# Kernel optimization log

Hardware: AMD Instinct MI355X
Metric: run time of the kernel (lower is better)

## Reference

```python
import jax, jax.numpy as jnp
import numpy as np

N_NODES = 50000
N_EDGES = 500000
MUL0, MUL1 = 16, 8          # multiplicities of 0e and 1o irreps (in == out)
DIM = MUL0 + 3 * MUL1       # 40
N_BASIS, MID = 10, 32
WNUM = MUL0*MUL0 + MUL1*MUL0 + MUL0*MUL1 + MUL1*MUL1  # 576
INV_SQRT3 = 1.0 / np.sqrt(3.0)  # wigner-3j normalization for l=1 paths
FAN_IN = MUL0 + MUL1        # paths into each output irrep: 16 + 8 = 24
A0 = np.sqrt(1.0 / FAN_IN)  # sqrt((2*0+1)/fan_in)
A1 = np.sqrt(3.0 / FAN_IN)  # sqrt((2*1+1)/fan_in)
LN_EPS = 1e-5


def setup_inputs() -> dict:
    key = jax.random.key(0)
    ks = jax.random.split(key, 8)
    return {
        "x": jax.random.normal(ks[0], (N_NODES, DIM), jnp.float32),
        "edge_sh": jax.random.normal(ks[1], (N_EDGES, 4), jnp.float32),
        "edge_length_embedded": jax.random.uniform(ks[2], (N_EDGES, N_BASIS), jnp.float32),
        "W1": jax.random.normal(ks[3], (N_BASIS, MID), jnp.float32),
        "W2": jax.random.normal(ks[4], (MID, WNUM), jnp.float32),
        "gamma": jnp.ones((DIM,), jnp.float32),
        "beta": jnp.zeros((DIM,), jnp.float32),
        "edge_src": jax.random.randint(ks[5], (N_EDGES,), 0, N_NODES),
        "edge_dst": jax.random.randint(ks[6], (N_EDGES,), 0, N_NODES),
        "avg_num_neighbors": 10,
    }


def reference(x, edge_sh, edge_length_embedded, W1, W2, gamma, beta,
              edge_src, edge_dst, avg_num_neighbors):
    # radial MLP -> per-edge tensor-product weights (e3nn FullyConnectedNet style)
    h = jax.nn.silu(edge_length_embedded @ W1 / jnp.sqrt(jnp.float32(N_BASIS)))
    w = h @ W2 / jnp.sqrt(jnp.float32(MID))              # [E, 576]

    # gather node features onto edges and split into irrep blocks
    xg = x[edge_src]                                     # [E, 40]
    s = xg[:, :MUL0]                                     # [E, 16]  scalars 0e
    v = xg[:, MUL0:].reshape(-1, MUL1, 3)                # [E, 8, 3] vectors 1o
    sh0 = edge_sh[:, 0]                                  # [E]
    sh1 = edge_sh[:, 1:4]                                # [E, 3]

    # split per-edge weights by tensor-product path
    o0, o1, o2 = MUL0*MUL0, MUL0*MUL0 + MUL1*MUL0, MUL0*MUL0 + MUL1*MUL0 + MUL0*MUL1
    W_ss0 = w[:, :o0].reshape(-1, MUL0, MUL0)            # 0e x 0e -> 0e
    W_vv0 = w[:, o0:o1].reshape(-1, MUL1, MUL0)          # 1o x 1o -> 0e
    W_sv1 = w[:, o1:o2].reshape(-1, MUL0, MUL1)          # 0e x 1o -> 1o
    W_vs1 = w[:, o2:].reshape(-1, MUL1, MUL1)            # 1o x 0e -> 1o

    # weighted Clebsch-Gordan tensor product (per edge)
    vdot = jnp.einsum('eui,ei->eu', v, sh1) * INV_SQRT3  # CG 1x1->0
    out0 = A0 * (jnp.einsum('euk,eu->ek', W_ss0, s * sh0[:, None])
                 + jnp.einsum('euk,eu->ek', W_vv0, vdot))            # [E, 16]
    out1 = A1 * INV_SQRT3 * (
        jnp.einsum('euk,eu->ek', W_sv1, s)[:, :, None] * sh1[:, None, :]
        + jnp.einsum('euk,eui->eki', W_vs1, v) * sh0[:, None, None])  # [E, 8, 3]
    edge_values = jnp.concatenate([out0, out1.reshape(-1, 3 * MUL1)], axis=1)

    # scatter-sum into destination nodes, degree normalization, layernorm
    node = jax.ops.segment_sum(edge_values, edge_dst, num_segments=N_NODES)
    node = node / jnp.sqrt(jnp.float32(avg_num_neighbors))
    mu = node.mean(axis=-1, keepdims=True)
    var = node.var(axis=-1, keepdims=True)
    return (node - mu) * jax.lax.rsqrt(var + LN_EPS) * gamma + beta
```

## Files before the change

kernel.cpp:

```cpp
#include <hip/hip_runtime.h>
#include <hip/hip_bf16.h>

#define N_NODES 50000
#define N_EDGES 500000
#define MUL0 16
#define MUL1 8
#define DIM 40
#define N_BASIS 10
#define MID 32
#define WNUM 576
#define SCAN_BLOCKS 196
#define N_GROUPS (N_EDGES / 16)

typedef __attribute__((ext_vector_type(8))) short bf16x8_t;
typedef __attribute__((ext_vector_type(4))) float f32x4_t;

__device__ __forceinline__ float bf2f(unsigned short u) {
  return __uint_as_float(((unsigned int)u) << 16);
}
__device__ __forceinline__ unsigned short f2bf(float f) {
  unsigned int x = __float_as_uint(f);
  unsigned int r = x + 0x7fffu + ((x >> 16) & 1u);
  return (unsigned short)(r >> 16);
}
__device__ __forceinline__ bool detect_bf16(const void* gamma) {
  return ((const unsigned int*)gamma)[0] == 0x3F803F80u;
}
template <bool BF16>
__device__ __forceinline__ float ld(const void* p, size_t i) {
  if (BF16) return bf2f(((const unsigned short*)p)[i]);
  return ((const float*)p)[i];
}

#define C_INV_SQRT10 0.31622776601683794f
#define C_INV_SQRT32 0.17677669529663687f
#define C_INV_SQRT3  0.5773502691896258f
#define C_A0C        0.20412414523193154f

__device__ __forceinline__ f32x4_t mfma16x16x32(bf16x8_t a, bf16x8_t b, f32x4_t c) {
  return __builtin_amdgcn_mfma_f32_16x16x32_bf16(a, b, c, 0, 0, 0);
}


__global__ __launch_bounds__(256) void hist_kernel(
    const int* __restrict__ edge_dst, int* __restrict__ cnt) {
  int e = blockIdx.x * 256 + threadIdx.x;
  if (e < N_EDGES) atomicAdd(&cnt[edge_dst[e]], 1);
}

__global__ __launch_bounds__(256) void scanA_kernel(
    const int* __restrict__ cnt, int* __restrict__ off, int* __restrict__ btot) {
  __shared__ int s[256];
  const int tid = threadIdx.x;
  const int i = blockIdx.x * 256 + tid;
  int v = (i < N_NODES) ? cnt[i] : 0;
  s[tid] = v;
  __syncthreads();
  for (int d = 1; d < 256; d <<= 1) {
    int t = (tid >= d) ? s[tid - d] : 0;
    __syncthreads();
    s[tid] += t;
    __syncthreads();
  }
  if (i < N_NODES) off[i] = s[tid] - v;
  if (tid == 255) btot[blockIdx.x] = s[255];
}

__global__ __launch_bounds__(256) void scanB_kernel(
    const int* __restrict__ btot, int* __restrict__ bbase) {
  __shared__ int s[256];
  const int tid = threadIdx.x;
  int v = (tid < SCAN_BLOCKS) ? btot[tid] : 0;
  s[tid] = v;
  __syncthreads();
  for (int d = 1; d < 256; d <<= 1) {
    int t = (tid >= d) ? s[tid - d] : 0;
    __syncthreads();
    s[tid] += t;
    __syncthreads();
  }
  if (tid < SCAN_BLOCKS) bbase[tid] = s[tid] - v;
}

__global__ __launch_bounds__(256) void scanC_kernel(
    int* __restrict__ off, const int* __restrict__ bbase) {
  const int i = blockIdx.x * 256 + threadIdx.x;
  if (i < N_NODES) off[i] += bbase[blockIdx.x];
}

__global__ __launch_bounds__(256) void pos_kernel(
    const int* __restrict__ edge_dst, const int* __restrict__ off,
    int* __restrict__ fill, int* __restrict__ epos) {
  int e = blockIdx.x * 256 + threadIdx.x;
  if (e >= N_EDGES) return;
  int d = edge_dst[e];
  epos[e] = off[d] + atomicAdd(&fill[d], 1);
}


template <bool BF16>
__device__ void edge_mfma_body(
    const void* __restrict__ x,
    const void* __restrict__ edge_sh,
    const void* __restrict__ elemb,
    const void* __restrict__ W1,
    const void* __restrict__ W2,
    const int* __restrict__ edge_src,
    const int* __restrict__ epos,
    unsigned short* __restrict__ ev,
    short* __restrict__ w2b, float* __restrict__ w1s, float* __restrict__ stg)
{
  const int tid = threadIdx.x;

  for (int i = tid; i < 36 * 512; i += 256) {
    int m = i / WNUM;
    int col = i - m * WNUM;
    int q = m >> 3, j = m & 7;
    int t = col >> 4, n = col & 15;
    short val;
    if (BF16) val = (short)((const unsigned short*)W2)[i];
    else      val = (short)f2bf(((const float*)W2)[i]);
    w2b[t * 512 + q * 128 + n * 8 + j] = val;
  }
  for (int i = tid; i < N_BASIS * MID; i += 256) w1s[i] = ld<BF16>(W1, i);
  __syncthreads();

  const int lane = tid & 63;
  const int wid  = tid >> 6;
  const int quad = lane >> 4;
  const int l16  = lane & 15;
  float* S = stg + wid * 832;

  for (int gi = blockIdx.x * 4 + wid; gi < N_GROUPS; gi += gridDim.x * 4) {
    const int e0 = gi * 16;
    __builtin_amdgcn_wave_barrier();

    const int posA = epos[e0 + (lane >> 2)];
    const int posB = (lane < 16) ? epos[e0 + lane] : 0;

    if (lane < 16) {
      if (BF16) {
        uint2 sw = *reinterpret_cast<const uint2*>(
            (const unsigned short*)edge_sh + (size_t)(e0 + lane) * 4);
        S[0 * 16 + lane] = __uint_as_float(sw.x << 16);
        S[1 * 16 + lane] = __uint_as_float(sw.x & 0xffff0000u);
        S[2 * 16 + lane] = __uint_as_float(sw.y << 16);
        S[3 * 16 + lane] = __uint_as_float(sw.y & 0xffff0000u);
      } else {
        float4 s4 = *reinterpret_cast<const float4*>(
            (const float*)edge_sh + (size_t)(e0 + lane) * 4);
        S[0 * 16 + lane] = s4.x; S[1 * 16 + lane] = s4.y;
        S[2 * 16 + lane] = s4.z; S[3 * 16 + lane] = s4.w;
      }
    }

    {
      const int src = edge_src[e0 + l16];
      if (BF16) {
        const uint4* xr = reinterpret_cast<const uint4*>(
            (const unsigned short*)x + (size_t)src * DIM);
        uint4 c = xr[quad];
        unsigned wv[4] = {c.x, c.y, c.z, c.w};
        #pragma unroll
        for (int p = 0; p < 4; ++p) {
          int col = quad * 8 + 2 * p;
          float lo = __uint_as_float(wv[p] << 16);
          float hi = __uint_as_float(wv[p] & 0xffff0000u);
          int off0 = (col < 16) ? (64 + col * 16) : (448 + (col - 16) * 16);
          int off1 = (col + 1 < 16) ? (64 + (col + 1) * 16) : (448 + (col - 15) * 16);
          S[off0 + l16] = lo;
          S[off1 + l16] = hi;
        }
        if (lane < 16) {
          uint4 c4 = xr[4];
          unsigned wv4[4] = {c4.x, c4.y, c4.z, c4.w};
          #pragma unroll
          for (int p = 0; p < 4; ++p) {
            int col = 32 + 2 * p;
            S[448 + (col - 16) * 16 + lane] = __uint_as_float(wv4[p] << 16);
            S[448 + (col - 15) * 16 + lane] = __uint_as_float(wv4[p] & 0xffff0000u);
          }
        }
      } else {
        const float4* xr = reinterpret_cast<const float4*>(
            (const float*)x + (size_t)src * DIM);
        #pragma unroll
        for (int cc = 0; cc < 2; ++cc) {
          int c = quad + cc * 4;
          float4 t = xr[c];
          float vv[4] = {t.x, t.y, t.z, t.w};
          #pragma unroll
          for (int p = 0; p < 4; ++p) {
            int col = 4 * c + p;
            int offp = (col < 16) ? (64 + col * 16) : (448 + (col - 16) * 16);
            S[offp + l16] = vv[p];
          }
        }
        if (quad < 2) {
          int c = 8 + quad;
          float4 t = xr[c];
          float vv[4] = {t.x, t.y, t.z, t.w};
          #pragma unroll
          for (int p = 0; p < 4; ++p) {
            int col = 4 * c + p;
            S[448 + (col - 16) * 16 + l16] = vv[p];
          }
        }
      }
    }
    __builtin_amdgcn_wave_barrier();

    #pragma unroll
    for (int p = 0; p < 2; ++p) {
      int idx = lane + p * 64;
      int u = idx >> 4, e = idx & 15;
      float vdv = (S[448 + (u * 3 + 0) * 16 + e] * S[16 + e] +
                   S[448 + (u * 3 + 1) * 16 + e] * S[32 + e] +
                   S[448 + (u * 3 + 2) * 16 + e] * S[48 + e]) * C_INV_SQRT3;
      S[320 + u * 16 + e] = vdv;
    }
    __builtin_amdgcn_wave_barrier();

    bf16x8_t af;
    {
      float eb[N_BASIS];
      if (BF16) {
        const unsigned short* er = (const unsigned short*)elemb + (size_t)(e0 + l16) * N_BASIS;
        #pragma unroll
        for (int p = 0; p < 5; ++p) {
          unsigned uv = *reinterpret_cast<const unsigned*>(er + p * 2);
          eb[2 * p]     = __uint_as_float(uv << 16);
          eb[2 * p + 1] = __uint_as_float(uv & 0xffff0000u);
        }
      } else {
        const float* er = (const float*)elemb + (size_t)(e0 + l16) * N_BASIS;
        #pragma unroll
        for (int p = 0; p < 5; ++p) {
          float2 fv = *reinterpret_cast<const float2*>(er + p * 2);
          eb[2 * p] = fv.x; eb[2 * p + 1] = fv.y;
        }
      }
      #pragma unroll
      for (int j = 0; j < 8; ++j) {
        int k = quad * 8 + j;
        float p = 0.f;
        #pragma unroll
        for (int b = 0; b < N_BASIS; ++b) p += eb[b] * w1s[b * MID + k];
        float z = p * C_INV_SQRT10;
        float hh = z / (1.f + __expf(-z)) * C_INV_SQRT32;
        af[j] = (short)f2bf(hh);
      }
    }

    f32x4_t s0 = *reinterpret_cast<const f32x4_t*>(&S[quad * 4]);

    f32x4_t out0 = {0.f, 0.f, 0.f, 0.f};
    f32x4_t tsv  = {0.f, 0.f, 0.f, 0.f};
    f32x4_t tv0  = {0.f, 0.f, 0.f, 0.f};
    f32x4_t tv1  = {0.f, 0.f, 0.f, 0.f};
    f32x4_t tv2  = {0.f, 0.f, 0.f, 0.f};
    const f32x4_t zero = {0.f, 0.f, 0.f, 0.f};
    const int usel = (l16 >> 3);

    #pragma unroll
    for (int t = 0; t < 16; ++t) {
      bf16x8_t bf = *reinterpret_cast<const bf16x8_t*>(&w2b[t * 512 + lane * 8]);
      f32x4_t D = mfma16x16x32(af, bf, zero);
      f32x4_t sv = *reinterpret_cast<const f32x4_t*>(&S[64 + t * 16 + quad * 4]);
      out0 += D * (sv * s0);
    }
    #pragma unroll
    for (int t = 0; t < 8; ++t) {
      bf16x8_t bf = *reinterpret_cast<const bf16x8_t*>(&w2b[(16 + t) * 512 + lane * 8]);
      f32x4_t D = mfma16x16x32(af, bf, zero);
      f32x4_t vdv = *reinterpret_cast<const f32x4_t*>(&S[320 + t * 16 + quad * 4]);
      out0 += D * vdv;
    }
    #pragma unroll
    for (int t = 0; t < 8; ++t) {
      bf16x8_t bf = *reinterpret_cast<const bf16x8_t*>(&w2b[(24 + t) * 512 + lane * 8]);
      f32x4_t D = mfma16x16x32(af, bf, zero);
      int u = 2 * t + usel;
      f32x4_t sv = *reinterpret_cast<const f32x4_t*>(&S[64 + u * 16 + quad * 4]);
      tsv += D * sv;
    }
    #pragma unroll
    for (int t = 0; t < 4; ++t) {
      bf16x8_t bf = *reinterpret_cast<const bf16x8_t*>(&w2b[(32 + t) * 512 + lane * 8]);
      f32x4_t D = mfma16x16x32(af, bf, zero);
      int u = 2 * t + usel;
      f32x4_t v0 = *reinterpret_cast<const f32x4_t*>(&S[448 + (u * 3 + 0) * 16 + quad * 4]);
      f32x4_t v1 = *reinterpret_cast<const f32x4_t*>(&S[448 + (u * 3 + 1) * 16 + quad * 4]);
      f32x4_t v2 = *reinterpret_cast<const f32x4_t*>(&S[448 + (u * 3 + 2) * 16 + quad * 4]);
      tv0 += D * v0; tv1 += D * v1; tv2 += D * v2;
    }

    #pragma unroll
    for (int r = 0; r < 4; ++r) {
      tsv[r] += __shfl_xor(tsv[r], 8, 64);
      tv0[r] += __shfl_xor(tv0[r], 8, 64);
      tv1[r] += __shfl_xor(tv1[r], 8, 64);
      tv2[r] += __shfl_xor(tv2[r], 8, 64);
    }
    __builtin_amdgcn_wave_barrier();

    #pragma unroll
    for (int r = 0; r < 4; ++r)
      S[64 + (quad * 4 + r) * 42 + l16] = C_A0C * out0[r];
    if (l16 < 8) {
      f32x4_t h1x = *reinterpret_cast<const f32x4_t*>(&S[16 + quad * 4]);
      f32x4_t h1y = *reinterpret_cast<const f32x4_t*>(&S[32 + quad * 4]);
      f32x4_t h1z = *reinterpret_cast<const f32x4_t*>(&S[48 + quad * 4]);
      #pragma unroll
      for (int r = 0; r < 4; ++r) {
        int rowb = 64 + (quad * 4 + r) * 42 + 16 + 3 * l16;
        S[rowb + 0] = C_A0C * (tsv[r] * h1x[r] + tv0[r] * s0[r]);
        S[rowb + 1] = C_A0C * (tsv[r] * h1y[r] + tv1[r] * s0[r]);
        S[rowb + 2] = C_A0C * (tsv[r] * h1z[r] + tv2[r] * s0[r]);
      }
    }
    __builtin_amdgcn_wave_barrier();

    {
      const int edge = lane >> 2, chunk = lane & 3;
      const float* rp = &S[64 + edge * 42 + chunk * 8];
      unsigned p0 = (unsigned)f2bf(rp[0]) | ((unsigned)f2bf(rp[1]) << 16);
      unsigned p1 = (unsigned)f2bf(rp[2]) | ((unsigned)f2bf(rp[3]) << 16);
      unsigned p2 = (unsigned)f2bf(rp[4]) | ((unsigned)f2bf(rp[5]) << 16);
      unsigned p3 = (unsigned)f2bf(rp[6]) | ((unsigned)f2bf(rp[7]) << 16);
      uint4 t; t.x = p0; t.y = p1; t.z = p2; t.w = p3;
      *reinterpret_cast<uint4*>(ev + (size_t)posA * DIM + chunk * 8) = t;
      if (lane < 16) {
        const float* rq = &S[64 + lane * 42 + 32];
        unsigned q0 = (unsigned)f2bf(rq[0]) | ((unsigned)f2bf(rq[1]) << 16);
        unsigned q1 = (unsigned)f2bf(rq[2]) | ((unsigned)f2bf(rq[3]) << 16);
        unsigned q2 = (unsigned)f2bf(rq[4]) | ((unsigned)f2bf(rq[5]) << 16);
        unsigned q3 = (unsigned)f2bf(rq[6]) | ((unsigned)f2bf(rq[7]) << 16);
        uint4 t2; t2.x = q0; t2.y = q1; t2.z = q2; t2.w = q3;
        *reinterpret_cast<uint4*>(ev + (size_t)posB * DIM + 32) = t2;
      }
    }
  }
}

__global__ __launch_bounds__(256, 3) void edge_mfma_kernel(
    const void* __restrict__ x,
    const void* __restrict__ edge_sh,
    const void* __restrict__ elemb,
    const void* __restrict__ W1,
    const void* __restrict__ W2,
    const void* __restrict__ gamma,
    const int* __restrict__ edge_src,
    const int* __restrict__ epos,
    unsigned short* __restrict__ ev)
{
  __shared__ __align__(16) short w2b[36 * 512];
  __shared__ __align__(16) float w1s[N_BASIS * MID];
  __shared__ __align__(16) float stg[4 * 832];

  if (detect_bf16(gamma))
    edge_mfma_body<true >(x, edge_sh, elemb, W1, W2, edge_src, epos, ev, w2b, w1s, stg);
  else
    edge_mfma_body<false>(x, edge_sh, elemb, W1, W2, edge_src, epos, ev, w2b, w1s, stg);
}


template <bool BF16>
__device__ __forceinline__ void node_body(
    const unsigned short* __restrict__ ev,
    const int* __restrict__ cnt,
    const int* __restrict__ off,
    const void* __restrict__ gamma,
    const void* __restrict__ beta,
    const int* __restrict__ avg,
    void* __restrict__ out, int n)
{
  const int c = cnt[n];
  const int o = off[n];
  float s[DIM];
  #pragma unroll
  for (int d = 0; d < DIM; ++d) s[d] = 0.f;

  const uint4* p = reinterpret_cast<const uint4*>(ev + (size_t)o * DIM);
  for (int j = 0; j < c; ++j) {
    #pragma unroll
    for (int q = 0; q < 5; ++q) {
      uint4 t = p[j * 5 + q];
      unsigned int wl[4] = {t.x, t.y, t.z, t.w};
      #pragma unroll
      for (int r = 0; r < 4; ++r) {
        s[q * 8 + 2 * r]     += __uint_as_float(wl[r] << 16);
        s[q * 8 + 2 * r + 1] += __uint_as_float(wl[r] & 0xffff0000u);
      }
    }
  }

  const float inv = rsqrtf((float)avg[0]);
  float mean = 0.f;
  #pragma unroll
  for (int d = 0; d < DIM; ++d) { s[d] *= inv; mean += s[d]; }
  mean *= (1.f / DIM);
  float var = 0.f;
  #pragma unroll
  for (int d = 0; d < DIM; ++d) { float dd = s[d] - mean; var += dd * dd; }
  var *= (1.f / DIM);
  const float r = rsqrtf(var + 1e-5f);

  if (BF16) {
    #pragma unroll
    for (int d = 0; d < DIM; ++d) {
      float y = (s[d] - mean) * r * ld<true>(gamma, d) + ld<true>(beta, d);
      ((unsigned short*)out)[(size_t)n * DIM + d] = f2bf(y);
    }
  } else {
    float4* op = reinterpret_cast<float4*>((float*)out + (size_t)n * DIM);
    #pragma unroll
    for (int q = 0; q < 10; ++q) {
      float4 t;
      t.x = (s[q*4+0] - mean) * r * ld<false>(gamma, q*4+0) + ld<false>(beta, q*4+0);
      t.y = (s[q*4+1] - mean) * r * ld<false>(gamma, q*4+1) + ld<false>(beta, q*4+1);
      t.z = (s[q*4+2] - mean) * r * ld<false>(gamma, q*4+2) + ld<false>(beta, q*4+2);
      t.w = (s[q*4+3] - mean) * r * ld<false>(gamma, q*4+3) + ld<false>(beta, q*4+3);
      op[q] = t;
    }
  }
}

__global__ __launch_bounds__(256) void node_kernel(
    const unsigned short* __restrict__ ev,
    const int* __restrict__ cnt,
    const int* __restrict__ off,
    const void* __restrict__ gamma,
    const void* __restrict__ beta,
    const int* __restrict__ avg,
    void* __restrict__ out)
{
  const int n = blockIdx.x * blockDim.x + threadIdx.x;
  if (n >= N_NODES) return;
  if (detect_bf16(gamma)) node_body<true >(ev, cnt, off, gamma, beta, avg, out, n);
  else                    node_body<false>(ev, cnt, off, gamma, beta, avg, out, n);
}

extern "C" void kernel_launch(void* const* d_in, const int* in_sizes, int n_in,
                              void* d_out, int out_size, void* d_ws, size_t ws_size,
                              hipStream_t stream) {
  const void* x       = d_in[0];
  const void* edge_sh = d_in[1];
  const void* elemb   = d_in[2];
  const void* W1      = d_in[3];
  const void* W2      = d_in[4];
  const void* gamma   = d_in[5];
  const void* beta    = d_in[6];
  const int* edge_src = (const int*)d_in[7];
  const int* edge_dst = (const int*)d_in[8];
  const int* avg      = (const int*)d_in[9];

  char* wsb = (char*)d_ws;
  unsigned short* ev = (unsigned short*)(wsb);
  int* epos  = (int*)(wsb + 40000000);
  int* cnt   = (int*)(wsb + 42000000);
  int* fill  = (int*)(wsb + 42200000);
  int* off   = (int*)(wsb + 42400000);
  int* btot  = (int*)(wsb + 42600000);
  int* bbase = (int*)(wsb + 42600800);

  hipMemsetAsync(cnt, 0, 400000, stream);

  const int EB = (N_EDGES + 255) / 256;
  hist_kernel <<<EB, 256, 0, stream>>>(edge_dst, cnt);
  scanA_kernel<<<SCAN_BLOCKS, 256, 0, stream>>>(cnt, off, btot);
  scanB_kernel<<<1, 256, 0, stream>>>(btot, bbase);
  scanC_kernel<<<SCAN_BLOCKS, 256, 0, stream>>>(off, bbase);
  pos_kernel  <<<EB, 256, 0, stream>>>(edge_dst, off, fill, epos);

  edge_mfma_kernel<<<768, 256, 0, stream>>>(x, edge_sh, elemb, W1, W2, gamma,
                                            edge_src, epos, ev);

  node_kernel<<<SCAN_BLOCKS, 256, 0, stream>>>(ev, cnt, off,
                                               gamma, beta, avg, d_out);
}
```

Before: 241.8 us.

## Fuse edge ranking into histogram and software-prefetch next edge group

The histogram kernel now records each edge's atomic rank, which removes the separate position kernel, its fill counters and one memset region. The edge kernel computes each destination slot as off[dst]+rank on the fly and prefetches the next group's gathered node features, spherical harmonics, embeddings and indices into registers while the current group computes. The bf16 path is replaced by a slow scalar per-edge fallback, which only matters if inputs are bf16. Prefetching raises register pressure, which may lower occupancy under the existing launch bounds.

Measured after the change: 279.3 us. +15.5%, slower.

```diff
diff --git a/kernel.cpp b/kernel.cpp
--- a/kernel.cpp
+++ b/kernel.cpp
@@ -41,11 +41,11 @@
   return __builtin_amdgcn_mfma_f32_16x16x32_bf16(a, b, c, 0, 0, 0);
 }
 
-
-__global__ __launch_bounds__(256) void hist_kernel(
-    const int* __restrict__ edge_dst, int* __restrict__ cnt) {
+__global__ __launch_bounds__(256) void rank_kernel(
+    const int* __restrict__ edge_dst, int* __restrict__ cnt,
+    int* __restrict__ rank) {
   int e = blockIdx.x * 256 + threadIdx.x;
-  if (e < N_EDGES) atomicAdd(&cnt[edge_dst[e]], 1);
+  if (e < N_EDGES) rank[e] = atomicAdd(&cnt[edge_dst[e]], 1);
 }
 
 __global__ __launch_bounds__(256) void scanA_kernel(
@@ -88,25 +88,69 @@
   if (i < N_NODES) off[i] += bbase[blockIdx.x];
 }
 
-__global__ __launch_bounds__(256) void pos_kernel(
-    const int* __restrict__ edge_dst, const int* __restrict__ off,
-    int* __restrict__ fill, int* __restrict__ epos) {
-  int e = blockIdx.x * 256 + threadIdx.x;
-  if (e >= N_EDGES) return;
-  int d = edge_dst[e];
-  epos[e] = off[d] + atomicAdd(&fill[d], 1);
-}
-
-
-template <bool BF16>
-__device__ void edge_mfma_body(
-    const void* __restrict__ x,
-    const void* __restrict__ edge_sh,
-    const void* __restrict__ elemb,
-    const void* __restrict__ W1,
-    const void* __restrict__ W2,
+
+__device__ void edge_scalar_bf16_one(
+    const unsigned short* __restrict__ xu, const unsigned short* __restrict__ shu,
+    const unsigned short* __restrict__ ebu, const unsigned short* __restrict__ W1u,
+    const unsigned short* __restrict__ W2u,
+    const int* __restrict__ edge_src, const int* __restrict__ edge_dst,
+    const int* __restrict__ rank, const int* __restrict__ off,
+    unsigned short* __restrict__ ev, int e)
+{
+  float ebv[N_BASIS];
+  for (int b = 0; b < N_BASIS; ++b) ebv[b] = bf2f(ebu[(size_t)e * N_BASIS + b]);
+  float h[MID];
+  for (int m = 0; m < MID; ++m) {
+    float p = 0.f;
+    for (int b = 0; b < N_BASIS; ++b) p += ebv[b] * bf2f(W1u[b * MID + m]);
+    float z = p * C_INV_SQRT10;
+    h[m] = z / (1.f + __expf(-z)) * C_INV_SQRT32;
+  }
+  const int src = edge_src[e];
+  float xv[DIM];
+  for (int d = 0; d < DIM; ++d) xv[d] = bf2f(xu[(size_t)src * DIM + d]);
+  float sh0 = bf2f(shu[(size_t)e*4+0]), sh1x = bf2f(shu[(size_t)e*4+1]),
+        sh1y = bf2f(shu[(size_t)e*4+2]), sh1z = bf2f(shu[(size_t)e*4+3]);
+  float vd[MUL1];
+  for (int u = 0; u < MUL1; ++u)
+    vd[u] = (xv[16+u*3]*sh1x + xv[17+u*3]*sh1y + xv[18+u*3]*sh1z) * C_INV_SQRT3;
+
+  auto wcol = [&](int j) {
+    float p = 0.f;
+    for (int m = 0; m < MID; ++m) p += h[m] * bf2f(W2u[m * WNUM + j]);
+    return p;
+  };
+  float out0[16]; for (int k = 0; k < 16; ++k) out0[k] = 0.f;
+  float tsv[8];   for (int k = 0; k < 8; ++k) tsv[k] = 0.f;
+  float tvs[24];  for (int t = 0; t < 24; ++t) tvs[t] = 0.f;
+  for (int u = 0; u < 16; ++u) { float c = xv[u]*sh0; for (int k = 0; k < 16; ++k) out0[k] += c*wcol(u*16+k); }
+  for (int u = 0; u < 8;  ++u) { for (int k = 0; k < 16; ++k) out0[k] += vd[u]*wcol(256+u*16+k); }
+  for (int u = 0; u < 16; ++u) { for (int k = 0; k < 8;  ++k) tsv[k] += xv[u]*wcol(384+u*8+k); }
+  for (int u = 0; u < 8;  ++u) { for (int k = 0; k < 8;  ++k) {
+      float w = wcol(512+u*8+k);
+      for (int i = 0; i < 3; ++i) tvs[k*3+i] += xv[16+u*3+i]*w; } }
+
+  const int pos = off[edge_dst[e]] + rank[e];
+  unsigned short* op = ev + (size_t)pos * DIM;
+  for (int k = 0; k < 16; ++k) op[k] = f2bf(C_A0C * out0[k]);
+  for (int k = 0; k < 8; ++k) {
+    op[16+k*3+0] = f2bf(C_A0C*(tsv[k]*sh1x + tvs[k*3+0]*sh0));
+    op[16+k*3+1] = f2bf(C_A0C*(tsv[k]*sh1y + tvs[k*3+1]*sh0));
+    op[16+k*3+2] = f2bf(C_A0C*(tsv[k]*sh1z + tvs[k*3+2]*sh0));
+  }
+}
+
+
+__device__ void edge_mfma_f32(
+    const float* __restrict__ x,
+    const float* __restrict__ edge_sh,
+    const float* __restrict__ elemb,
+    const float* __restrict__ W1,
+    const float* __restrict__ W2,
     const int* __restrict__ edge_src,
-    const int* __restrict__ epos,
+    const int* __restrict__ edge_dst,
+    const int* __restrict__ rank,
+    const int* __restrict__ off,
     unsigned short* __restrict__ ev,
     short* __restrict__ w2b, float* __restrict__ w1s, float* __restrict__ stg)
 {
@@ -117,12 +161,9 @@
     int col = i - m * WNUM;
     int q = m >> 3, j = m & 7;
     int t = col >> 4, n = col & 15;
-    short val;
-    if (BF16) val = (short)((const unsigned short*)W2)[i];
-    else      val = (short)f2bf(((const float*)W2)[i]);
-    w2b[t * 512 + q * 128 + n * 8 + j] = val;
-  }
-  for (int i = tid; i < N_BASIS * MID; i += 256) w1s[i] = ld<BF16>(W1, i);
+    w2b[t * 512 + q * 128 + n * 8 + j] = (short)f2bf(W2[i]);
+  }
+  for (int i = tid; i < N_BASIS * MID; i += 256) w1s[i] = W1[i];
   __syncthreads();
 
   const int lane = tid & 63;
@@ -130,84 +171,89 @@
   const int quad = lane >> 4;
   const int l16  = lane & 15;
   float* S = stg + wid * 832;
-
-  for (int gi = blockIdx.x * 4 + wid; gi < N_GROUPS; gi += gridDim.x * 4) {
+  const int stride = gridDim.x * 4;
+
+  float4 pc0 = {0,0,0,0}, pc1 = {0,0,0,0}, pc2 = {0,0,0,0}, psh = {0,0,0,0};
+  float peb[N_BASIS];
+  int pposA = 0, pposB = 0;
+
+  int gi = blockIdx.x * 4 + wid;
+  if (gi >= N_GROUPS) return;
+
+  {
     const int e0 = gi * 16;
+    const int eA = e0 + (lane >> 2);
+    pposA = off[edge_dst[eA]] + rank[eA];
+    if (lane < 16) {
+      const int eB = e0 + lane;
+      pposB = off[edge_dst[eB]] + rank[eB];
+      psh = *reinterpret_cast<const float4*>(edge_sh + (size_t)eB * 4);
+    }
+    const int src = edge_src[e0 + l16];
+    const float4* xr = reinterpret_cast<const float4*>(x + (size_t)src * DIM);
+    pc0 = xr[quad]; pc1 = xr[quad + 4];
+    if (quad < 2) pc2 = xr[8 + quad];
+    const float* er = elemb + (size_t)(e0 + l16) * N_BASIS;
+    #pragma unroll
+    for (int p = 0; p < 5; ++p) {
+      float2 f = *reinterpret_cast<const float2*>(er + 2 * p);
+      peb[2 * p] = f.x; peb[2 * p + 1] = f.y;
+    }
+  }
+
+  for (; gi < N_GROUPS; gi += stride) {
+    const int e0 = gi * 16;
+
+    const int posA = pposA, posB = pposB;
+    const float4 c0 = pc0, c1 = pc1, c2 = pc2, sh4 = psh;
+    float eb[N_BASIS];
+    #pragma unroll
+    for (int b = 0; b < N_BASIS; ++b) eb[b] = peb[b];
+
     __builtin_amdgcn_wave_barrier();
 
-    const int posA = epos[e0 + (lane >> 2)];
-    const int posB = (lane < 16) ? epos[e0 + lane] : 0;
-
     if (lane < 16) {
-      if (BF16) {
-        uint2 sw = *reinterpret_cast<const uint2*>(
-            (const unsigned short*)edge_sh + (size_t)(e0 + lane) * 4);
-        S[0 * 16 + lane] = __uint_as_float(sw.x << 16);
-        S[1 * 16 + lane] = __uint_as_float(sw.x & 0xffff0000u);
-        S[2 * 16 + lane] = __uint_as_float(sw.y << 16);
-        S[3 * 16 + lane] = __uint_as_float(sw.y & 0xffff0000u);
-      } else {
-        float4 s4 = *reinterpret_cast<const float4*>(
-            (const float*)edge_sh + (size_t)(e0 + lane) * 4);
-        S[0 * 16 + lane] = s4.x; S[1 * 16 + lane] = s4.y;
-        S[2 * 16 + lane] = s4.z; S[3 * 16 + lane] = s4.w;
+      S[0 + lane] = sh4.x; S[16 + lane] = sh4.y;
+      S[32 + lane] = sh4.z; S[48 + lane] = sh4.w;
+    }
+    {
+      const float v0[4] = {c0.x, c0.y, c0.z, c0.w};
+      const float v1[4] = {c1.x, c1.y, c1.z, c1.w};
+      #pragma unroll
+      for (int p = 0; p < 4; ++p) {
+        S[64  + (4 * quad + p) * 16 + l16] = v0[p];
+        S[448 + (4 * quad + p) * 16 + l16] = v1[p];
       }
-    }
-
+      if (quad < 2) {
+        const float v2[4] = {c2.x, c2.y, c2.z, c2.w};
+        #pragma unroll
+        for (int p = 0; p < 4; ++p)
+          S[448 + (16 + 4 * quad + p) * 16 + l16] = v2[p];
+      }
+    }
+
+    const int gn = gi + stride;
+    const int en = (gn < N_GROUPS) ? gn * 16 : 0;
+    const int eAn = en + (lane >> 2);
+    const int dstA = edge_dst[eAn];
+    const int rkA  = rank[eAn];
+    int dstB = 0, rkB = 0;
+    if (lane < 16) {
+      const int eBn = en + lane;
+      dstB = edge_dst[eBn];
+      rkB  = rank[eBn];
+      psh = *reinterpret_cast<const float4*>(edge_sh + (size_t)eBn * 4);
+    }
+    const int srcn = edge_src[en + l16];
     {
-      const int src = edge_src[e0 + l16];
-      if (BF16) {
-        const uint4* xr = reinterpret_cast<const uint4*>(
-            (const unsigned short*)x + (size_t)src * DIM);
-        uint4 c = xr[quad];
-        unsigned wv[4] = {c.x, c.y, c.z, c.w};
-        #pragma unroll
-        for (int p = 0; p < 4; ++p) {
-          int col = quad * 8 + 2 * p;
-          float lo = __uint_as_float(wv[p] << 16);
-          float hi = __uint_as_float(wv[p] & 0xffff0000u);
-          int off0 = (col < 16) ? (64 + col * 16) : (448 + (col - 16) * 16);
-          int off1 = (col + 1 < 16) ? (64 + (col + 1) * 16) : (448 + (col - 15) * 16);
-          S[off0 + l16] = lo;
-          S[off1 + l16] = hi;
-        }
-        if (lane < 16) {
-          uint4 c4 = xr[4];
-          unsigned wv4[4] = {c4.x, c4.y, c4.z, c4.w};
-          #pragma unroll
-          for (int p = 0; p < 4; ++p) {
-            int col = 32 + 2 * p;
-            S[448 + (col - 16) * 16 + lane] = __uint_as_float(wv4[p] << 16);
-            S[448 + (col - 15) * 16 + lane] = __uint_as_float(wv4[p] & 0xffff0000u);
-          }
-        }
-      } else {
-        const float4* xr = reinterpret_cast<const float4*>(
-            (const float*)x + (size_t)src * DIM);
-        #pragma unroll
-        for (int cc = 0; cc < 2; ++cc) {
-          int c = quad + cc * 4;
-          float4 t = xr[c];
-          float vv[4] = {t.x, t.y, t.z, t.w};
-          #pragma unroll
-          for (int p = 0; p < 4; ++p) {
-            int col = 4 * c + p;
-            int offp = (col < 16) ? (64 + col * 16) : (448 + (col - 16) * 16);
-            S[offp + l16] = vv[p];
-          }
-        }
-        if (quad < 2) {
-          int c = 8 + quad;
-          float4 t = xr[c];
-          float vv[4] = {t.x, t.y, t.z, t.w};
-          #pragma unroll
-          for (int p = 0; p < 4; ++p) {
-            int col = 4 * c + p;
-            S[448 + (col - 16) * 16 + l16] = vv[p];
-          }
-        }
+      const float* er = elemb + (size_t)(en + l16) * N_BASIS;
+      #pragma unroll
+      for (int p = 0; p < 5; ++p) {
+        float2 f = *reinterpret_cast<const float2*>(er + 2 * p);
+        peb[2 * p] = f.x; peb[2 * p + 1] = f.y;
       }
     }
+
     __builtin_amdgcn_wave_barrier();
 
     #pragma unroll
@@ -222,34 +268,23 @@
     __builtin_amdgcn_wave_barrier();
 
     bf16x8_t af;
+    #pragma unroll
+    for (int j = 0; j < 8; ++j) {
+      int k = quad * 8 + j;
+      float p = 0.f;
+      #pragma unroll
+      for (int b = 0; b < N_BASIS; ++b) p += eb[b] * w1s[b * MID + k];
+      float z = p * C_INV_SQRT10;
+      float hh = z / (1.f + __expf(-z)) * C_INV_SQRT32;
+      af[j] = (short)f2bf(hh);
+    }
+
+    pposA = off[dstA] + rkA;
+    if (lane < 16) pposB = off[dstB] + rkB;
     {
-      float eb[N_BASIS];
-      if (BF16) {
-        const unsigned short* er = (const unsigned short*)elemb + (size_t)(e0 + l16) * N_BASIS;
-        #pragma unroll
-        for (int p = 0; p < 5; ++p) {
-          unsigned uv = *reinterpret_cast<const unsigned*>(er + p * 2);
-          eb[2 * p]     = __uint_as_float(uv << 16);
-          eb[2 * p + 1] = __uint_as_float(uv & 0xffff0000u);
-        }
-      } else {
-        const float* er = (const float*)elemb + (size_t)(e0 + l16) * N_BASIS;
-        #pragma unroll
-        for (int p = 0; p < 5; ++p) {
-          float2 fv = *reinterpret_cast<const float2*>(er + p * 2);
-          eb[2 * p] = fv.x; eb[2 * p + 1] = fv.y;
-        }
-      }
-      #pragma unroll
-      for (int j = 0; j < 8; ++j) {
-        int k = quad * 8 + j;
-        float p = 0.f;
-        #pragma unroll
-        for (int b = 0; b < N_BASIS; ++b) p += eb[b] * w1s[b * MID + k];
-        float z = p * C_INV_SQRT10;
-        float hh = z / (1.f + __expf(-z)) * C_INV_SQRT32;
-        af[j] = (short)f2bf(hh);
-      }
+      const float4* xr = reinterpret_cast<const float4*>(x + (size_t)srcn * DIM);
+      pc0 = xr[quad]; pc1 = xr[quad + 4];
+      if (quad < 2) pc2 = xr[8 + quad];
     }
 
     f32x4_t s0 = *reinterpret_cast<const f32x4_t*>(&S[quad * 4]);
@@ -351,17 +386,26 @@
     const void* __restrict__ W2,
     const void* __restrict__ gamma,
     const int* __restrict__ edge_src,
-    const int* __restrict__ epos,
+    const int* __restrict__ edge_dst,
+    const int* __restrict__ rank,
+    const int* __restrict__ off,
     unsigned short* __restrict__ ev)
 {
   __shared__ __align__(16) short w2b[36 * 512];
   __shared__ __align__(16) float w1s[N_BASIS * MID];
   __shared__ __align__(16) float stg[4 * 832];
 
-  if (detect_bf16(gamma))
-    edge_mfma_body<true >(x, edge_sh, elemb, W1, W2, edge_src, epos, ev, w2b, w1s, stg);
-  else
-    edge_mfma_body<false>(x, edge_sh, elemb, W1, W2, edge_src, epos, ev, w2b, w1s, stg);
+  if (detect_bf16(gamma)) {
+    for (int e = blockIdx.x * 256 + threadIdx.x; e < N_EDGES; e += gridDim.x * 256)
+      edge_scalar_bf16_one((const unsigned short*)x, (const unsigned short*)edge_sh,
+                           (const unsigned short*)elemb, (const unsigned short*)W1,
+                           (const unsigned short*)W2, edge_src, edge_dst, rank, off,
+                           ev, e);
+    return;
+  }
+  edge_mfma_f32((const float*)x, (const float*)edge_sh, (const float*)elemb,
+                (const float*)W1, (const float*)W2,
+                edge_src, edge_dst, rank, off, ev, w2b, w1s, stg);
 }
 
 
@@ -457,24 +501,22 @@
 
   char* wsb = (char*)d_ws;
   unsigned short* ev = (unsigned short*)(wsb);
-  int* epos  = (int*)(wsb + 40000000);
+  int* rank  = (int*)(wsb + 40000000);
   int* cnt   = (int*)(wsb + 42000000);
-  int* fill  = (int*)(wsb + 42200000);
-  int* off   = (int*)(wsb + 42400000);
-  int* btot  = (int*)(wsb + 42600000);
-  int* bbase = (int*)(wsb + 42600800);
-
-  hipMemsetAsync(cnt, 0, 400000, stream);
+  int* off   = (int*)(wsb + 42200000);
+  int* btot  = (int*)(wsb + 42400000);
+  int* bbase = (int*)(wsb + 42400800);
+
+  hipMemsetAsync(cnt, 0, 200000, stream);
 
   const int EB = (N_EDGES + 255) / 256;
-  hist_kernel <<<EB, 256, 0, stream>>>(edge_dst, cnt);
+  rank_kernel <<<EB, 256, 0, stream>>>(edge_dst, cnt, rank);
   scanA_kernel<<<SCAN_BLOCKS, 256, 0, stream>>>(cnt, off, btot);
   scanB_kernel<<<1, 256, 0, stream>>>(btot, bbase);
   scanC_kernel<<<SCAN_BLOCKS, 256, 0, stream>>>(off, bbase);
-  pos_kernel  <<<EB, 256, 0, stream>>>(edge_dst, off, fill, epos);
 
   edge_mfma_kernel<<<768, 256, 0, stream>>>(x, edge_sh, elemb, W1, W2, gamma,
-                                            edge_src, epos, ev);
+                                            edge_src, edge_dst, rank, off, ev);
 
   node_kernel<<<SCAN_BLOCKS, 256, 0, stream>>>(ev, cnt, off,
                                                gamma, beta, avg, d_out);
```
